# Kernel tuning notes

Hardware: AMD Instinct MI355X
Metric: run time of the kernel (lower is better)

The kernel has to match this reference:

```python
import jax, jax.numpy as jnp
import numpy as np

D_MODEL, NHEAD = 256, 8
HEAD_DIM = D_MODEL // NHEAD  # 32, also the conv group count


def layer_norm(x, w, b, eps=1e-5):
    mu = jnp.mean(x, axis=-1, keepdims=True)
    var = jnp.var(x, axis=-1, keepdims=True)
    return (x - mu) * jax.lax.rsqrt(var + eps) * w + b


def setup_inputs() -> dict:
    key = jax.random.key(0)
    ks = jax.random.split(key, 12)
    b, H, W = 4, 120, 160
    L = H * W  # 19200; 'self' path requires L == H*W
    d, h = D_MODEL, NHEAD
    s = 0.05
    p = lambda i, shape: jax.random.normal(ks[i], shape, jnp.float32) * s
    return {
        "x": jax.random.normal(ks[0], (b, L, d), jnp.float32),
        "source": jax.random.normal(ks[1], (b, L, d), jnp.float32),
        "Wq": p(2, (d, d)), "Wk": p(3, (d, d)), "Wv": p(4, (d, d)),
        "Wmerge": p(5, (d, d)),
        "Wmlp1": p(6, (2 * d, 2 * d)), "Wmlp2": p(7, (2 * d, d)),
        "ln1_w": jnp.ones((d,), jnp.float32), "ln1_b": jnp.zeros((d,), jnp.float32),
        "ln2_w": jnp.ones((d,), jnp.float32), "ln2_b": jnp.zeros((d,), jnp.float32),
        "Wdown": p(8, (2 * d, 64)), "Wup": p(9, (64, d)),
        "fc_w": p(10, (9, 3 * h)), "fc_b": jnp.zeros((9,), jnp.float32),
        "dep_w": p(11, (d, 9, 3, 3)),  # torch OIHW layout, groups=32 (O/g=8, I/g=9)
        "dep_b": jnp.zeros((d,), jnp.float32),
        "rate": jnp.full((1,), 0.5, jnp.float32),
        "H": H, "W": W,
    }


def reference(x, source, Wq, Wk, Wv, Wmerge, Wmlp1, Wmlp2,
              ln1_w, ln1_b, ln2_w, ln2_b, Wdown, Wup,
              fc_w, fc_b, dep_w, dep_b, rate, H, W):
    # name == 'self' path is hardcoded (conv branch active)
    b, L, d = x.shape
    h, hd = NHEAD, HEAD_DIM
    S = source.shape[1]

    q = (x @ Wq).reshape(b, L, h, hd)
    k = (source @ Wk).reshape(b, S, h, hd)
    v = (source @ Wv).reshape(b, S, h, hd)

    # ---- conv branch ----
    # [b, L, h, 3*hd] -> [b, L, 3h, hd] -> [b, 3h, L, hd]
    f_all = jnp.concatenate([q, k, v], axis=-1).reshape(b, L, 3 * h, hd)
    f_all = jnp.transpose(f_all, (0, 2, 1, 3))
    # 1x1 conv 3h -> 9 over (L, hd) 'spatial' grid
    f9 = jnp.einsum('oc,bcld->bold', fc_w, f_all) + fc_b[None, :, None, None]
    # [b, 9, L, hd] -> [b, hd, 9, L] -> [b, 9*hd, H, W]
    f_conv = jnp.transpose(f9, (0, 3, 1, 2)).reshape(b, 9 * hd, H, W)
    out_conv = jax.lax.conv_general_dilated(
        f_conv, dep_w, window_strides=(1, 1), padding=((1, 1), (1, 1)),
        feature_group_count=hd, dimension_numbers=('NCHW', 'OIHW', 'NCHW'))
    out_conv = out_conv + dep_b[None, :, None, None]
    out_conv = jnp.transpose(out_conv, (0, 2, 3, 1)).reshape(b, L, d)

    # ---- linear attention (elu+1 feature map), O(N) ----
    Qf = jax.nn.elu(q) + 1.0
    Kf = jax.nn.elu(k) + 1.0
    v_len = jnp.float32(S)
    vals = v / v_len
    KV = jnp.einsum('bshd,bshv->bhdv', Kf, vals)
    Z = 1.0 / (jnp.einsum('blhd,bhd->blh', Qf, Kf.sum(axis=1)) + 1e-6)
    message = jnp.einsum('blhd,bhdv,blh->blhv', Qf, KV, Z) * v_len

    # ---- merge / norm / MLP / adapter ----
    message = message.reshape(b, L, d) @ Wmerge
    message = layer_norm(message, ln1_w, ln1_b)
    cat1 = jnp.concatenate([x, message], axis=2)
    message = jax.nn.relu(cat1 @ Wmlp1) @ Wmlp2
    message = layer_norm(message, ln2_w, ln2_b)

    cat2 = jnp.concatenate([x, message], axis=2)
    up = jax.nn.relu(cat2 @ Wdown) @ Wup
    message = message + up * 0.1
    message = message + rate * out_conv
    return x + message
```

## Files before the change

### kernel.cpp

```cpp
#include <hip/hip_runtime.h>
#include <stdint.h>

#define LL 19200
#define NBATCH 4
#define NROWS (NBATCH * LL)
#define HH 120
#define WW 160

typedef short bhalf8 __attribute__((ext_vector_type(8)));
typedef float f32x4 __attribute__((ext_vector_type(4)));

__device__ __forceinline__ float bfbits2f(uint32_t u) { union { uint32_t i; float f; } c; c.i = u << 16; return c.f; }
__device__ __forceinline__ float bf2f(uint16_t h) { return bfbits2f((uint32_t)h); }
__device__ __forceinline__ uint16_t f2bf(float f) {
    union { float f; uint32_t i; } c; c.f = f;
    return (uint16_t)((c.i + 0x7FFFu + ((c.i >> 16) & 1u)) >> 16);
}
__device__ __forceinline__ uint32_t pk2(uint16_t a, uint16_t b) { return (uint32_t)a | ((uint32_t)b << 16); }
__device__ __forceinline__ float elup1(float x) { return x > 0.f ? x + 1.f : expf(x); }

__device__ __forceinline__ uint4 pack8f(const float* p) {
    float4 lo = *(const float4*)p; float4 hi = *(const float4*)(p + 4);
    uint4 s;
    s.x = pk2(f2bf(lo.x), f2bf(lo.y)); s.y = pk2(f2bf(lo.z), f2bf(lo.w));
    s.z = pk2(f2bf(hi.x), f2bf(hi.y)); s.w = pk2(f2bf(hi.z), f2bf(hi.w));
    return s;
}

__device__ __forceinline__ void gll16(const void* g, void* l) {
    __builtin_amdgcn_global_load_lds((const __attribute__((address_space(1))) uint32_t*)g,
                                     (__attribute__((address_space(3))) uint32_t*)l, 16, 0, 0);
}

__global__ __launch_bounds__(256)
void prep_all(const float* __restrict__ Wq, const float* __restrict__ Wk,
              const float* __restrict__ Wv, const float* __restrict__ Wm,
              const float* __restrict__ Wm1, const float* __restrict__ Wm2,
              const float* __restrict__ Wd, const float* __restrict__ Wu,
              uint16_t* __restrict__ wq, uint16_t* __restrict__ wk,
              uint16_t* __restrict__ wvv, uint16_t* __restrict__ wm,
              uint16_t* __restrict__ wm1, uint16_t* __restrict__ wm2,
              uint16_t* __restrict__ wd, uint16_t* __restrict__ wu) {
    __shared__ float ts[64][65];
    const int tid = threadIdx.x;
    int blk = blockIdx.x;
    const float* s; uint16_t* d; int K, N, t;
    if (blk < 64)        { int w = blk >> 4; t = blk & 15;
                           s = w == 0 ? Wq : w == 1 ? Wk : w == 2 ? Wv : Wm;
                           d = w == 0 ? wq : w == 1 ? wk : w == 2 ? wvv : wm;
                           K = 256; N = 256; }
    else if (blk < 128)  { s = Wm1; d = wm1; K = 512; N = 512; t = blk - 64; }
    else if (blk < 160)  { s = Wm2; d = wm2; K = 512; N = 256; t = blk - 128; }
    else if (blk < 168)  { s = Wd;  d = wd;  K = 512; N = 64;  t = blk - 160; }
    else                 { s = Wu;  d = wu;  K = 64;  N = 256; t = blk - 168; }
    const int ntk = K >> 6;
    const int tn = t / ntk, tk = t - tn * ntk;
    const int c = tid & 63, r4 = tid >> 6;
#pragma unroll
    for (int i = 0; i < 16; ++i) {
        int r = r4 * 16 + i;
        ts[r][c] = s[(long)(tk * 64 + r) * N + tn * 64 + c];
    }
    __syncthreads();
#pragma unroll
    for (int i = 0; i < 16; ++i) {
        int rr = r4 * 16 + i;
        d[(long)(tn * 64 + rr) * K + tk * 64 + c] = f2bf(ts[c][rr]);
    }
}

#define EPI_NONE 0
#define EPI_RELU 1
#define EPI_LN 2
#define EPI_FINAL 3

template<int BN, int K, int MODE_A, int EPI>
__global__ __launch_bounds__(512)
void gemm_big(const float* __restrict__ A0f, const uint16_t* __restrict__ A0b,
              const uint16_t* __restrict__ A1b,
              const uint16_t* __restrict__ Wt,
              uint16_t* __restrict__ outb, float* __restrict__ outf, int outW,
              uint16_t* __restrict__ sideout,
              const float* __restrict__ lnw, const float* __restrict__ lnb,
              const float* __restrict__ xres, const uint16_t* __restrict__ xresb,
              const uint16_t* __restrict__ msg2res,
              const uint16_t* __restrict__ convres, const float* __restrict__ ratep)
{
    constexpr int WCOLS = BN / 64;
    constexpr int WROWS = 8 / WCOLS;
    constexpr int MT = 128 / (WROWS * 16);
    constexpr int ASZ = 128 * 32;
    constexpr int BSZ = BN * 32;
    __shared__ __align__(16) uint16_t a_sm[2 * ASZ];
    __shared__ __align__(16) uint16_t b_sm[2 * BSZ];
    const int tid = threadIdx.x;
    const int lane = tid & 63;
    const int wv = tid >> 6;
    const int wr = wv / WCOLS, wc = wv % WCOLS;
    const long row0 = (long)blockIdx.x * 128;
    const int col0 = blockIdx.y * BN;
    const int l15 = lane & 15, lk = lane >> 4;

    f32x4 acc[MT][4];
#pragma unroll
    for (int m = 0; m < MT; ++m)
#pragma unroll
        for (int n = 0; n < 4; ++n) acc[m][n] = (f32x4){0.f, 0.f, 0.f, 0.f};

    const int sr = tid >> 2;
    const int sc = (tid & 3) * 8;
    const long argA = row0 + sr;

    auto stageAB = [&](int buf, int k0) {
        uint16_t* ab = a_sm + buf * ASZ;
        uint16_t* bb = b_sm + buf * BSZ;
        if (MODE_A == 0) {
            gll16(A0b + argA * (long)K + k0 + sc, ab + wv * 512);
        } else if (MODE_A == 1) {
            uint4 stg = pack8f(A0f + argA * (long)K + k0 + sc);
            *(uint4*)&ab[sr * 32 + sc] = stg;
            if (sideout) *(uint4*)(sideout + argA * (long)K + k0 + sc) = stg;
        } else if (MODE_A == 2) {
            if (k0 < 256) *(uint4*)&ab[sr * 32 + sc] = pack8f(A0f + argA * 256 + k0 + sc);
            else          gll16(A1b + argA * 256 + (k0 - 256) + sc, ab + wv * 512);
        } else {
            const uint16_t* srcp = (k0 < 256) ? (A0b + argA * 256 + k0 + sc)
                                              : (A1b + argA * 256 + (k0 - 256) + sc);
            gll16(srcp, ab + wv * 512);
        }
        if (BN == 256) {
            gll16(Wt + (long)(col0 + sr) * K + k0 + sc, bb + wv * 512);
            gll16(Wt + (long)(col0 + 128 + sr) * K + k0 + sc, bb + 4096 + wv * 512);
        } else {
            if (tid < 256) gll16(Wt + (long)(col0 + sr) * K + k0 + sc, bb + wv * 512);
        }
    };

    auto comp = [&](int buf) {
        const uint16_t* ab = a_sm + buf * ASZ;
        const uint16_t* bb = b_sm + buf * BSZ;
        bhalf8 af[MT];
#pragma unroll
        for (int m = 0; m < MT; ++m)
            af[m] = *(const bhalf8*)&ab[(wr * MT * 16 + m * 16 + l15) * 32 + lk * 8];
#pragma unroll
        for (int n = 0; n < 4; ++n) {
            bhalf8 bfr = *(const bhalf8*)&bb[(wc * 64 + n * 16 + l15) * 32 + lk * 8];
#pragma unroll
            for (int m = 0; m < MT; ++m)
                acc[m][n] = __builtin_amdgcn_mfma_f32_16x16x32_bf16(af[m], bfr, acc[m][n], 0, 0, 0);
        }
    };

    stageAB(0, 0);
    __syncthreads();
    int cur = 0;
#pragma unroll
    for (int k0 = 32; k0 < K; k0 += 32) {
        stageAB(cur ^ 1, k0);
        comp(cur);
        __syncthreads();
        cur ^= 1;
    }
    comp(cur);

    const int cl = l15;
    const int rg4 = lk * 4;

    if constexpr (EPI == EPI_LN) {
        __shared__ float red_s[4][128];
        __shared__ float red_ss[4][128];
#pragma unroll
        for (int m = 0; m < MT; ++m)
#pragma unroll
            for (int j = 0; j < 4; ++j) {
                float p = 0.f, pp = 0.f;
#pragma unroll
                for (int n = 0; n < 4; ++n) { float v = acc[m][n][j]; p += v; pp += v * v; }
#pragma unroll
                for (int msk = 1; msk < 16; msk <<= 1) { p += __shfl_xor(p, msk, 64); pp += __shfl_xor(pp, msk, 64); }
                if (cl == 0) {
                    int lr = wr * 64 + m * 16 + rg4 + j;
                    red_s[wc][lr] = p; red_ss[wc][lr] = pp;
                }
            }
        __syncthreads();
#pragma unroll
        for (int m = 0; m < MT; ++m)
#pragma unroll
            for (int j = 0; j < 4; ++j) {
                int lr = wr * 64 + m * 16 + rg4 + j;
                float s = red_s[0][lr] + red_s[1][lr] + red_s[2][lr] + red_s[3][lr];
                float ss = red_ss[0][lr] + red_ss[1][lr] + red_ss[2][lr] + red_ss[3][lr];
                float mu = s * (1.f / 256.f);
                float var = ss * (1.f / 256.f) - mu * mu;
                float rstd = rsqrtf(var + 1e-5f);
                long rowg = row0 + lr;
#pragma unroll
                for (int n = 0; n < 4; ++n) {
                    int col = wc * 64 + n * 16 + cl;
                    float vv = (acc[m][n][j] - mu) * rstd * lnw[col] + lnb[col];
                    outb[rowg * (long)outW + col] = f2bf(vv);
                }
            }
    } else if constexpr (EPI == EPI_FINAL) {
        float rate = ratep[0];
#pragma unroll
        for (int m = 0; m < MT; ++m)
#pragma unroll
            for (int j = 0; j < 4; ++j) {
                long rowg = row0 + wr * MT * 16 + m * 16 + rg4 + j;
                int bb2 = (int)(rowg / LL);
                int ll = (int)(rowg - (long)bb2 * LL);
#pragma unroll
                for (int n = 0; n < 4; ++n) {
                    int col = wc * 64 + n * 16 + cl;
                    long o = rowg * 256 + col;
                    float xv = xresb ? bf2f(xresb[o]) : xres[o];
                    float m2 = bf2f(msg2res[o]);
                    float cv = bf2f(convres[((long)(bb2 * 256 + col)) * LL + ll]);
                    outf[o] = xv + m2 + 0.1f * acc[m][n][j] + rate * cv;
                }
            }
    } else {
#pragma unroll
        for (int m = 0; m < MT; ++m)
#pragma unroll
            for (int j = 0; j < 4; ++j) {
                long rowg = row0 + wr * MT * 16 + m * 16 + rg4 + j;
#pragma unroll
                for (int n = 0; n < 4; ++n) {
                    int col = col0 + wc * 64 + n * 16 + cl;
                    float vv = acc[m][n][j];
                    if (EPI == EPI_RELU) vv = vv > 0.f ? vv : 0.f;
                    outb[rowg * (long)outW + col] = f2bf(vv);
                }
            }
    }
}

__global__ __launch_bounds__(256)
void kv_partial(const uint16_t* __restrict__ kb, const uint16_t* __restrict__ vb,
                float* __restrict__ part) {
    __shared__ float kf_sm[32][33];
    __shared__ float v_sm[32][36];
    const int tid = threadIdx.x;
    const int bh = blockIdx.y, b = bh >> 3, h = bh & 7;
    const int s0 = blockIdx.x * 256;
    const int d = tid >> 3, vg = tid & 7;
    const int sl = tid >> 3, e4 = (tid & 7) * 4;
    float a0 = 0.f, a1 = 0.f, a2 = 0.f, a3 = 0.f, aKs = 0.f;
    for (int it = 0; it < 8; ++it) {
        long base = ((long)(b * LL + s0 + it * 32 + sl)) * 256 + h * 32 + e4;
        uint2 kk = *(const uint2*)(kb + base);
        uint2 vv = *(const uint2*)(vb + base);
        kf_sm[sl][e4 + 0] = elup1(bfbits2f(kk.x & 0xFFFFu));
        kf_sm[sl][e4 + 1] = elup1(bfbits2f(kk.x >> 16));
        kf_sm[sl][e4 + 2] = elup1(bfbits2f(kk.y & 0xFFFFu));
        kf_sm[sl][e4 + 3] = elup1(bfbits2f(kk.y >> 16));
        float4 vf;
        vf.x = bfbits2f(vv.x & 0xFFFFu); vf.y = bfbits2f(vv.x >> 16);
        vf.z = bfbits2f(vv.y & 0xFFFFu); vf.w = bfbits2f(vv.y >> 16);
        *(float4*)&v_sm[sl][e4] = vf;
        __syncthreads();
#pragma unroll 8
        for (int s = 0; s < 32; ++s) {
            float kf = kf_sm[s][d];
            aKs += kf;
            float4 v4 = *(const float4*)&v_sm[s][vg * 4];
            a0 += kf * v4.x; a1 += kf * v4.y; a2 += kf * v4.z; a3 += kf * v4.w;
        }
        __syncthreads();
    }
    long pb = ((long)(blockIdx.x * 32 + bh)) * 1056;
    part[pb + d * 32 + vg * 4 + 0] = a0;
    part[pb + d * 32 + vg * 4 + 1] = a1;
    part[pb + d * 32 + vg * 4 + 2] = a2;
    part[pb + d * 32 + vg * 4 + 3] = a3;
    if (vg == 0) part[pb + 1024 + d] = aKs;
}

__global__ __launch_bounds__(256)
void kv_final(const float* __restrict__ part, float* __restrict__ KVg, float* __restrict__ Ksum) {
    const int bh = blockIdx.x, tid = threadIdx.x;
    for (int idx = tid; idx < 1056; idx += 256) {
        float s = 0.f;
        for (int c = 0; c < 75; ++c) s += part[((long)(c * 32 + bh)) * 1056 + idx];
        if (idx < 1024) KVg[bh * 1024 + idx] = s;
        else Ksum[bh * 32 + idx - 1024] = s;
    }
}

__global__ __launch_bounds__(256)
void attn_mfma(const uint16_t* __restrict__ qb, const float* __restrict__ KVg,
               const float* __restrict__ Ksum, uint16_t* __restrict__ msgout) {
    const int tid = threadIdx.x;
    const int lane = tid & 63;
    const int wv = tid >> 6;
    const long l0 = (long)blockIdx.x * 64;
    const int b = (int)(l0 / LL);
    const int l15 = lane & 15, lk = lane >> 4;
#pragma unroll
    for (int hi = 0; hi < 2; ++hi) {
        const int h = wv * 2 + hi;
        const float* kvb = KVg + ((long)(b * 8 + h)) * 1024;
        const float* ksb = Ksum + (b * 8 + h) * 32;
        bhalf8 B0, B1;
        float ks[8];
#pragma unroll
        for (int i = 0; i < 8; ++i) {
            int k = lk * 8 + i;
            B0[i] = (short)f2bf(kvb[k * 32 + l15]);
            B1[i] = (short)f2bf(kvb[k * 32 + 16 + l15]);
            ks[i] = ksb[k];
        }
#pragma unroll
        for (int rt = 0; rt < 4; ++rt) {
            long row = l0 + rt * 16 + l15;
            uint4 qv = *(const uint4*)(qb + row * 256 + h * 32 + lk * 8);
            float qf[8];
            qf[0] = elup1(bfbits2f(qv.x & 0xFFFFu)); qf[1] = elup1(bfbits2f(qv.x >> 16));
            qf[2] = elup1(bfbits2f(qv.y & 0xFFFFu)); qf[3] = elup1(bfbits2f(qv.y >> 16));
            qf[4] = elup1(bfbits2f(qv.z & 0xFFFFu)); qf[5] = elup1(bfbits2f(qv.z >> 16));
            qf[6] = elup1(bfbits2f(qv.w & 0xFFFFu)); qf[7] = elup1(bfbits2f(qv.w >> 16));
            bhalf8 A;
#pragma unroll
            for (int i = 0; i < 8; ++i) A[i] = (short)f2bf(qf[i]);
            float p = qf[0]*ks[0] + qf[1]*ks[1] + qf[2]*ks[2] + qf[3]*ks[3]
                    + qf[4]*ks[4] + qf[5]*ks[5] + qf[6]*ks[6] + qf[7]*ks[7];
            p += __shfl_xor(p, 16, 64);
            p += __shfl_xor(p, 32, 64);
            f32x4 d0 = (f32x4){0.f,0.f,0.f,0.f}, d1 = (f32x4){0.f,0.f,0.f,0.f};
            d0 = __builtin_amdgcn_mfma_f32_16x16x32_bf16(A, B0, d0, 0, 0, 0);
            d1 = __builtin_amdgcn_mfma_f32_16x16x32_bf16(A, B1, d1, 0, 0, 0);
#pragma unroll
            for (int j = 0; j < 4; ++j) {
                int orl = lk * 4 + j;
                float zr = __shfl(p, orl, 64);
                float Z = 1.f / (zr + 1e-6f);
                long orow = l0 + rt * 16 + orl;
                msgout[orow * 256 + h * 32 + l15]      = f2bf(d0[j] * Z);
                msgout[orow * 256 + h * 32 + 16 + l15] = f2bf(d1[j] * Z);
            }
        }
    }
}

__global__ __launch_bounds__(256)
void f9_kernel(const uint16_t* __restrict__ qb, const uint16_t* __restrict__ kb,
               const uint16_t* __restrict__ vb, const float* __restrict__ fcw,
               const float* __restrict__ fcb, uint16_t* __restrict__ fconv) {
    __shared__ __align__(16) uint16_t sm[3 * 32 * 256];
    char* smb = (char*)sm;
    const int tid = threadIdx.x;
    const int b = blockIdx.y;
    const int l0 = blockIdx.x * 32;
    for (int idx = tid; idx < 3072; idx += 256) {
        int tsr = idx >> 10, row = (idx >> 5) & 31, c = idx & 31;
        const uint16_t* src = tsr == 0 ? qb : (tsr == 1 ? kb : vb);
        uint4 v = *(const uint4*)(src + ((long)(b * LL + l0 + row)) * 256 + c * 8);
        int boff = (c * 16) ^ ((row & 7) << 4);
        *(uint4*)(smb + (tsr * 32 + row) * 512 + boff) = v;
    }
    __syncthreads();
    const int li = tid & 31, g = tid >> 5;
    float acc[9][4];
#pragma unroll
    for (int o = 0; o < 9; ++o) {
        float bv = fcb[o];
#pragma unroll
        for (int j = 0; j < 4; ++j) acc[o][j] = bv;
    }
    const int swz = (li & 7) << 4;
#pragma unroll
    for (int h = 0; h < 8; ++h) {
        float f[3][4];
#pragma unroll
        for (int s = 0; s < 3; ++s) {
            int boff = (h * 64 + g * 8) ^ swz;
            uint2 r = *(const uint2*)(smb + (s * 32 + li) * 512 + boff);
            f[s][0] = bfbits2f(r.x & 0xFFFFu); f[s][1] = bfbits2f(r.x >> 16);
            f[s][2] = bfbits2f(r.y & 0xFFFFu); f[s][3] = bfbits2f(r.y >> 16);
        }
#pragma unroll
        for (int o = 0; o < 9; ++o) {
            float w0 = fcw[o * 24 + 3 * h + 0];
            float w1 = fcw[o * 24 + 3 * h + 1];
            float w2 = fcw[o * 24 + 3 * h + 2];
#pragma unroll
            for (int j = 0; j < 4; ++j)
                acc[o][j] += w0 * f[0][j] + w1 * f[1][j] + w2 * f[2][j];
        }
    }
    const long ob = (long)(b * 288) * LL + l0 + li;
#pragma unroll
    for (int j = 0; j < 4; ++j) {
        int dp = g * 4 + j;
#pragma unroll
        for (int o = 0; o < 9; ++o)
            fconv[ob + (long)(dp * 9 + o) * LL] = f2bf(acc[o][j]);
    }
}

__global__ __launch_bounds__(256)
void dwconv2(const uint16_t* __restrict__ fconv, const float* __restrict__ depw,
             const float* __restrict__ depb, uint16_t* __restrict__ convout) {
    __shared__ __align__(16) uint16_t in_sm[9][26][48];
    __shared__ float w_sm[8][81];
    __shared__ float b_sm2[8];
    const int tid = threadIdx.x;
    const int bg = blockIdx.z, b = bg >> 5, g = bg & 31;
    const int y0 = blockIdx.y * 24;
    const int x0 = blockIdx.x * 32;
    for (int idx = tid; idx < 648; idx += 256)
        w_sm[idx / 81][idx % 81] = depw[(long)(g * 8) * 81 + idx];
    if (tid < 8) b_sm2[tid] = depb[g * 8 + tid];
    for (int rIdx = tid; rIdx < 234; rIdx += 256) {
        int i = rIdx / 26, r = rIdx - i * 26;
        int yy = y0 + r - 1;
        uint16_t* dst = &in_sm[i][r][0];
        if (yy >= 0 && yy < HH) {
            const uint16_t* rp = fconv + ((long)(b * 288 + g * 9 + i)) * LL + yy * WW;
            *(uint4*)&dst[8]  = *(const uint4*)(rp + x0);
            *(uint4*)&dst[16] = *(const uint4*)(rp + x0 + 8);
            *(uint4*)&dst[24] = *(const uint4*)(rp + x0 + 16);
            *(uint4*)&dst[32] = *(const uint4*)(rp + x0 + 24);
            dst[7]  = (x0 > 0) ? rp[x0 - 1] : (uint16_t)0;
            dst[40] = (x0 + 32 < WW) ? rp[x0 + 32] : (uint16_t)0;
        } else {
            uint4 z = {0, 0, 0, 0};
            *(uint4*)&dst[8] = z; *(uint4*)&dst[16] = z;
            *(uint4*)&dst[24] = z; *(uint4*)&dst[32] = z;
            dst[7] = 0; dst[40] = 0;
        }
    }
    __syncthreads();
    const int xi = tid & 7, m = (tid >> 3) & 7, ys = tid >> 6;
    float acc[6][4];
    float bias = b_sm2[m];
#pragma unroll
    for (int r = 0; r < 6; ++r)
#pragma unroll
        for (int o = 0; o < 4; ++o) acc[r][o] = bias;
    for (int i = 0; i < 9; ++i) {
        float w[9];
#pragma unroll
        for (int t = 0; t < 9; ++t) w[t] = w_sm[m][i * 9 + t];
#pragma unroll
        for (int rr = 0; rr < 8; ++rr) {
            const uint16_t* rowb = &in_sm[i][ys * 6 + rr][4 + xi * 4];
            uint2 lo = *(const uint2*)rowb;
            uint2 hi = *(const uint2*)(rowb + 4);
            uint32_t ex = *(const uint32_t*)(rowb + 8);
            float f[6];
            f[0] = bfbits2f(lo.y >> 16);
            f[1] = bfbits2f(hi.x & 0xFFFFu);
            f[2] = bfbits2f(hi.x >> 16);
            f[3] = bfbits2f(hi.y & 0xFFFFu);
            f[4] = bfbits2f(hi.y >> 16);
            f[5] = bfbits2f(ex & 0xFFFFu);
#pragma unroll
            for (int ky = 0; ky < 3; ++ky) {
                int ro = rr - ky;
                if (ro >= 0 && ro < 6) {
#pragma unroll
                    for (int o = 0; o < 4; ++o)
                        acc[ro][o] += w[ky * 3 + 0] * f[o] + w[ky * 3 + 1] * f[o + 1] + w[ky * 3 + 2] * f[o + 2];
                }
            }
        }
    }
    long chbase = ((long)(b * 256 + g * 8 + m)) * LL;
#pragma unroll
    for (int rl = 0; rl < 6; ++rl) {
        int y = y0 + ys * 6 + rl;
        uint2 st;
        st.x = pk2(f2bf(acc[rl][0]), f2bf(acc[rl][1]));
        st.y = pk2(f2bf(acc[rl][2]), f2bf(acc[rl][3]));
        *(uint2*)(convout + chbase + (long)y * WW + x0 + xi * 4) = st;
    }
}

extern "C" void kernel_launch(void* const* d_in, const int* in_sizes, int n_in,
                              void* d_out, int out_size, void* d_ws, size_t ws_size,
                              hipStream_t stream) {
    (void)in_sizes; (void)n_in; (void)out_size;
    const float* x      = (const float*)d_in[0];
    const float* src    = (const float*)d_in[1];
    const float* Wq     = (const float*)d_in[2];
    const float* Wk     = (const float*)d_in[3];
    const float* Wv     = (const float*)d_in[4];
    const float* Wmerge = (const float*)d_in[5];
    const float* Wmlp1  = (const float*)d_in[6];
    const float* Wmlp2  = (const float*)d_in[7];
    const float* ln1w   = (const float*)d_in[8];
    const float* ln1b   = (const float*)d_in[9];
    const float* ln2w   = (const float*)d_in[10];
    const float* ln2b   = (const float*)d_in[11];
    const float* Wdown  = (const float*)d_in[12];
    const float* Wup    = (const float*)d_in[13];
    const float* fcw    = (const float*)d_in[14];
    const float* fcb    = (const float*)d_in[15];
    const float* depw   = (const float*)d_in[16];
    const float* depb   = (const float*)d_in[17];
    const float* rate   = (const float*)d_in[18];

    char* ws = (char*)d_ws;
    const size_t SZ_NB = (size_t)NROWS * 256 * 2;
    const size_t O_Q = 0;
    const size_t O_K = SZ_NB;
    const size_t O_V = 2 * SZ_NB;
    const size_t O_FCONV = 3 * SZ_NB;
    const size_t O_CONVOUT = O_FCONV + (size_t)NBATCH * 288 * LL * 2;
    const size_t O_PART = O_CONVOUT + SZ_NB;
    const size_t O_KV = O_PART + (size_t)75 * 32 * 1056 * 4;
    const size_t O_KS = O_KV + (size_t)32 * 1024 * 4;
    const size_t O_WT = O_KS + (size_t)32 * 32 * 4;
    const size_t O_XB = O_WT + 704512 * 2 + 1024;
    const size_t O_SRCB = O_XB + SZ_NB;
    const size_t NEED = O_SRCB + SZ_NB;

    uint16_t* qB      = (uint16_t*)(ws + O_Q);
    uint16_t* kB      = (uint16_t*)(ws + O_K);
    uint16_t* vB      = (uint16_t*)(ws + O_V);
    uint16_t* fconv   = (uint16_t*)(ws + O_FCONV);
    uint16_t* convout = (uint16_t*)(ws + O_CONVOUT);
    float*    part    = (float*)(ws + O_PART);
    float*    KVg     = (float*)(ws + O_KV);
    float*    Ksg     = (float*)(ws + O_KS);
    uint16_t* wt_q    = (uint16_t*)(ws + O_WT);
    uint16_t* wt_k    = wt_q + 256 * 256;
    uint16_t* wt_v    = wt_k + 256 * 256;
    uint16_t* wt_m    = wt_v + 256 * 256;
    uint16_t* wt_m1   = wt_m + 256 * 256;
    uint16_t* wt_m2   = wt_m1 + 512 * 512;
    uint16_t* wt_d    = wt_m2 + 512 * 256;
    uint16_t* wt_u    = wt_d + 512 * 64;
    uint16_t* xb      = (uint16_t*)(ws + O_XB);
    uint16_t* srcb    = (uint16_t*)(ws + O_SRCB);
    uint16_t* msgattn = kB;
    uint16_t* msgB    = vB;
    uint16_t* hidden  = qB;
    uint16_t* msg2    = fconv;
    uint16_t* h2      = (uint16_t*)(ws + O_PART);

    const bool big = ws_size >= NEED;

    prep_all<<<172, 256, 0, stream>>>(Wq, Wk, Wv, Wmerge, Wmlp1, Wmlp2, Wdown, Wup,
                                      wt_q, wt_k, wt_v, wt_m, wt_m1, wt_m2, wt_d, wt_u);

    const dim3 g600(NROWS / 128, 1);
    gemm_big<256, 256, 1, EPI_NONE><<<g600, 512, 0, stream>>>(x, nullptr, nullptr, wt_q, qB, nullptr, 256,
        big ? xb : nullptr, nullptr, nullptr, nullptr, nullptr, nullptr, nullptr, nullptr);
    gemm_big<256, 256, 1, EPI_NONE><<<g600, 512, 0, stream>>>(src, nullptr, nullptr, wt_k, kB, nullptr, 256,
        big ? srcb : nullptr, nullptr, nullptr, nullptr, nullptr, nullptr, nullptr, nullptr);
    if (big) {
        gemm_big<256, 256, 0, EPI_NONE><<<g600, 512, 0, stream>>>(nullptr, srcb, nullptr, wt_v, vB, nullptr, 256,
            nullptr, nullptr, nullptr, nullptr, nullptr, nullptr, nullptr, nullptr);
    } else {
        gemm_big<256, 256, 1, EPI_NONE><<<g600, 512, 0, stream>>>(src, nullptr, nullptr, wt_v, vB, nullptr, 256,
            nullptr, nullptr, nullptr, nullptr, nullptr, nullptr, nullptr, nullptr);
    }
    kv_partial<<<dim3(75, 32), 256, 0, stream>>>(kB, vB, part);
    kv_final<<<32, 256, 0, stream>>>(part, KVg, Ksg);
    f9_kernel<<<dim3(LL / 32, NBATCH), 256, 0, stream>>>(qB, kB, vB, fcw, fcb, fconv);
    dwconv2<<<dim3(5, 5, 128), 256, 0, stream>>>(fconv, depw, depb, convout);
    attn_mfma<<<NROWS / 64, 256, 0, stream>>>(qB, KVg, Ksg, msgattn);
    gemm_big<256, 256, 0, EPI_LN><<<g600, 512, 0, stream>>>(nullptr, msgattn, nullptr, wt_m, msgB, nullptr, 256,
        nullptr, ln1w, ln1b, nullptr, nullptr, nullptr, nullptr, nullptr);
    if (big) {
        gemm_big<256, 512, 3, EPI_RELU><<<dim3(NROWS / 128, 2), 512, 0, stream>>>(nullptr, xb, msgB, wt_m1, hidden, nullptr, 512,
            nullptr, nullptr, nullptr, nullptr, nullptr, nullptr, nullptr, nullptr);
    } else {
        gemm_big<256, 512, 2, EPI_RELU><<<dim3(NROWS / 128, 2), 512, 0, stream>>>(x, nullptr, msgB, wt_m1, hidden, nullptr, 512,
            nullptr, nullptr, nullptr, nullptr, nullptr, nullptr, nullptr, nullptr);
    }
    gemm_big<256, 512, 0, EPI_LN><<<g600, 512, 0, stream>>>(nullptr, hidden, nullptr, wt_m2, msg2, nullptr, 256,
        nullptr, ln2w, ln2b, nullptr, nullptr, nullptr, nullptr, nullptr);
    if (big) {
        gemm_big<64, 512, 3, EPI_RELU><<<g600, 512, 0, stream>>>(nullptr, xb, msg2, wt_d, h2, nullptr, 64,
            nullptr, nullptr, nullptr, nullptr, nullptr, nullptr, nullptr, nullptr);
    } else {
        gemm_big<64, 512, 2, EPI_RELU><<<g600, 512, 0, stream>>>(x, nullptr, msg2, wt_d, h2, nullptr, 64,
            nullptr, nullptr, nullptr, nullptr, nullptr, nullptr, nullptr, nullptr);
    }
    gemm_big<256, 64, 0, EPI_FINAL><<<g600, 512, 0, stream>>>(nullptr, h2, nullptr, wt_u, nullptr, (float*)d_out, 256,
        nullptr, nullptr, nullptr, x, big ? xb : nullptr, msg2, convout, rate);
}
```

Before: 856.3 us.

## Pipeline GEMM k-loop with raw barriers, stage epilogue stores, pre-convert inputs

For GEMMs whose A operand is bf16 loaded via global_load_lds, the k-loop now uses explicit vmcnt waits and raw s_barrier so the next tile's loads stay in flight while the current tile computes. Epilogues (plain, ReLU, LayerNorm) now stage results through shared memory and write coalesced 16-byte rows instead of scattered 2-byte stores. A separate conversion kernel turns x and source to bf16 up front so the Q/K/V GEMMs all read bf16 directly. The MLP1 grid is transposed so the two column blocks of a row tile run next to each other for better A reuse in cache. The added conversion pass, the extra barriers and the hand-tuned waitcnt counts add cost and fragility.

```diff
diff --git a/kernel.cpp b/kernel.cpp
--- a/kernel.cpp
+++ b/kernel.cpp
@@ -30,6 +30,22 @@
 __device__ __forceinline__ void gll16(const void* g, void* l) {
     __builtin_amdgcn_global_load_lds((const __attribute__((address_space(1))) uint32_t*)g,
                                      (__attribute__((address_space(3))) uint32_t*)l, 16, 0, 0);
+}
+
+__device__ __forceinline__ void barrier_raw() {
+    asm volatile("" ::: "memory");
+    __builtin_amdgcn_s_barrier();
+    asm volatile("" ::: "memory");
+}
+
+__global__ __launch_bounds__(256)
+void conv_bf16(const float* __restrict__ a, const float* __restrict__ b,
+               uint16_t* __restrict__ oa, uint16_t* __restrict__ ob) {
+    const float* s = blockIdx.y ? b : a;
+    uint16_t* d = blockIdx.y ? ob : oa;
+    long i = ((long)blockIdx.x * 256 + threadIdx.x) * 16;
+    *(uint4*)(d + i)     = pack8f(s + i);
+    *(uint4*)(d + i + 8) = pack8f(s + i + 8);
 }
 
 __global__ __launch_bounds__(256)
@@ -74,7 +90,7 @@
 #define EPI_LN 2
 #define EPI_FINAL 3
 
-template<int BN, int K, int MODE_A, int EPI>
+template<int BN, int K, int MODE_A, int EPI, int COLX>
 __global__ __launch_bounds__(512)
 void gemm_big(const float* __restrict__ A0f, const uint16_t* __restrict__ A0b,
               const uint16_t* __restrict__ A1b,
@@ -91,14 +107,17 @@
     constexpr int MT = 128 / (WROWS * 16);
     constexpr int ASZ = 128 * 32;
     constexpr int BSZ = BN * 32;
-    __shared__ __align__(16) uint16_t a_sm[2 * ASZ];
-    __shared__ __align__(16) uint16_t b_sm[2 * BSZ];
+    constexpr int NSTEP = K / 32;
+    constexpr bool PIPE = (MODE_A == 0 || MODE_A == 3);
+    __shared__ __align__(16) uint16_t smem[2 * ASZ + 2 * BSZ];
+    uint16_t* a_sm = smem;
+    uint16_t* b_sm = smem + 2 * ASZ;
     const int tid = threadIdx.x;
     const int lane = tid & 63;
     const int wv = tid >> 6;
     const int wr = wv / WCOLS, wc = wv % WCOLS;
-    const long row0 = (long)blockIdx.x * 128;
-    const int col0 = blockIdx.y * BN;
+    const long row0 = (long)(COLX ? blockIdx.y : blockIdx.x) * 128;
+    const int col0 = (COLX ? blockIdx.x : blockIdx.y) * BN;
     const int l15 = lane & 15, lk = lane >> 4;
 
     f32x4 acc[MT][4];
@@ -152,58 +171,44 @@
         }
     };
 
-    stageAB(0, 0);
+    if constexpr (PIPE) {
+        stageAB(0, 0);
+#pragma unroll
+        for (int t = 0; t < NSTEP; ++t) {
+            if (t + 1 < NSTEP) {
+                stageAB((t + 1) & 1, (t + 1) * 32);
+                if constexpr (BN == 256) {
+                    asm volatile("s_waitcnt vmcnt(3)" ::: "memory");
+                } else {
+                    if (wv < 4) asm volatile("s_waitcnt vmcnt(2)" ::: "memory");
+                    else        asm volatile("s_waitcnt vmcnt(1)" ::: "memory");
+                }
+            } else {
+                asm volatile("s_waitcnt vmcnt(0)" ::: "memory");
+            }
+            barrier_raw();
+            comp(t & 1);
+            barrier_raw();
+        }
+    } else {
+        stageAB(0, 0);
+        __syncthreads();
+        int cur = 0;
+#pragma unroll
+        for (int k0 = 32; k0 < K; k0 += 32) {
+            stageAB(cur ^ 1, k0);
+            comp(cur);
+            __syncthreads();
+            cur ^= 1;
+        }
+        comp(cur);
+    }
     __syncthreads();
-    int cur = 0;
-#pragma unroll
-    for (int k0 = 32; k0 < K; k0 += 32) {
-        stageAB(cur ^ 1, k0);
-        comp(cur);
-        __syncthreads();
-        cur ^= 1;
-    }
-    comp(cur);
 
     const int cl = l15;
     const int rg4 = lk * 4;
 
-    if constexpr (EPI == EPI_LN) {
-        __shared__ float red_s[4][128];
-        __shared__ float red_ss[4][128];
-#pragma unroll
-        for (int m = 0; m < MT; ++m)
-#pragma unroll
-            for (int j = 0; j < 4; ++j) {
-                float p = 0.f, pp = 0.f;
-#pragma unroll
-                for (int n = 0; n < 4; ++n) { float v = acc[m][n][j]; p += v; pp += v * v; }
-#pragma unroll
-                for (int msk = 1; msk < 16; msk <<= 1) { p += __shfl_xor(p, msk, 64); pp += __shfl_xor(pp, msk, 64); }
-                if (cl == 0) {
-                    int lr = wr * 64 + m * 16 + rg4 + j;
-                    red_s[wc][lr] = p; red_ss[wc][lr] = pp;
-                }
-            }
-        __syncthreads();
-#pragma unroll
-        for (int m = 0; m < MT; ++m)
-#pragma unroll
-            for (int j = 0; j < 4; ++j) {
-                int lr = wr * 64 + m * 16 + rg4 + j;
-                float s = red_s[0][lr] + red_s[1][lr] + red_s[2][lr] + red_s[3][lr];
-                float ss = red_ss[0][lr] + red_ss[1][lr] + red_ss[2][lr] + red_ss[3][lr];
-                float mu = s * (1.f / 256.f);
-                float var = ss * (1.f / 256.f) - mu * mu;
-                float rstd = rsqrtf(var + 1e-5f);
-                long rowg = row0 + lr;
-#pragma unroll
-                for (int n = 0; n < 4; ++n) {
-                    int col = wc * 64 + n * 16 + cl;
-                    float vv = (acc[m][n][j] - mu) * rstd * lnw[col] + lnb[col];
-                    outb[rowg * (long)outW + col] = f2bf(vv);
-                }
-            }
-    } else if constexpr (EPI == EPI_FINAL) {
+    if constexpr (EPI == EPI_FINAL) {
         float rate = ratep[0];
 #pragma unroll
         for (int m = 0; m < MT; ++m)
@@ -222,20 +227,78 @@
                     outf[o] = xv + m2 + 0.1f * acc[m][n][j] + rate * cv;
                 }
             }
-    } else {
+        return;
+    }
+
+    float mu_r[MT][4], rs_r[MT][4];
+    float lw[4], lb[4];
+    if constexpr (EPI == EPI_LN) {
+        float* red_s  = (float*)smem;
+        float* red_ss = red_s + 512;
 #pragma unroll
         for (int m = 0; m < MT; ++m)
 #pragma unroll
             for (int j = 0; j < 4; ++j) {
-                long rowg = row0 + wr * MT * 16 + m * 16 + rg4 + j;
-#pragma unroll
-                for (int n = 0; n < 4; ++n) {
-                    int col = col0 + wc * 64 + n * 16 + cl;
-                    float vv = acc[m][n][j];
-                    if (EPI == EPI_RELU) vv = vv > 0.f ? vv : 0.f;
-                    outb[rowg * (long)outW + col] = f2bf(vv);
+                float p = 0.f, pp = 0.f;
+#pragma unroll
+                for (int n = 0; n < 4; ++n) { float v = acc[m][n][j]; p += v; pp += v * v; }
+#pragma unroll
+                for (int msk = 1; msk < 16; msk <<= 1) { p += __shfl_xor(p, msk, 64); pp += __shfl_xor(pp, msk, 64); }
+                if (cl == 0) {
+                    int lr = wr * 64 + m * 16 + rg4 + j;
+                    red_s[wc * 128 + lr] = p; red_ss[wc * 128 + lr] = pp;
                 }
             }
+        __syncthreads();
+#pragma unroll
+        for (int m = 0; m < MT; ++m)
+#pragma unroll
+            for (int j = 0; j < 4; ++j) {
+                int lr = wr * 64 + m * 16 + rg4 + j;
+                float s  = red_s[lr] + red_s[128 + lr] + red_s[256 + lr] + red_s[384 + lr];
+                float ss = red_ss[lr] + red_ss[128 + lr] + red_ss[256 + lr] + red_ss[384 + lr];
+                float mu = s * (1.f / 256.f);
+                float var = ss * (1.f / 256.f) - mu * mu;
+                mu_r[m][j] = mu;
+                rs_r[m][j] = rsqrtf(var + 1e-5f);
+            }
+#pragma unroll
+        for (int n = 0; n < 4; ++n) {
+            lw[n] = lnw[wc * 64 + n * 16 + cl];
+            lb[n] = lnb[wc * 64 + n * 16 + cl];
+        }
+        __syncthreads();
+    }
+
+    constexpr int CST = BN + 8;
+    uint16_t* stg = (EPI == EPI_LN) ? (smem + 2048) : smem;
+    constexpr int ROWS = (BN == 256) ? 32 : 128;
+    constexpr int GPR = BN / 8;
+#pragma unroll
+    for (int m = 0; m < MT; ++m) {
+        __syncthreads();
+#pragma unroll
+        for (int j = 0; j < 4; ++j) {
+            int lr = wr * 16 + rg4 + j;
+#pragma unroll
+            for (int n = 0; n < 4; ++n) {
+                float v = acc[m][n][j];
+                if constexpr (EPI == EPI_RELU) v = v > 0.f ? v : 0.f;
+                if constexpr (EPI == EPI_LN)   v = (v - mu_r[m][j]) * rs_r[m][j] * lw[n] + lb[n];
+                stg[lr * CST + wc * 64 + n * 16 + cl] = f2bf(v);
+            }
+        }
+        __syncthreads();
+#pragma unroll
+        for (int it = 0; it < (ROWS * GPR + 511) / 512; ++it) {
+            int flat = it * 512 + tid;
+            if (flat < ROWS * GPR) {
+                int lr = flat / GPR, g = flat % GPR;
+                long grow = (BN == 256) ? (row0 + (lr >> 4) * 64 + m * 16 + (lr & 15))
+                                        : (row0 + lr);
+                *(uint4*)(outb + grow * (long)outW + col0 + g * 8) = *(const uint4*)&stg[lr * CST + g * 8];
+            }
+        }
     }
 }
 
@@ -550,15 +613,20 @@
                                       wt_q, wt_k, wt_v, wt_m, wt_m1, wt_m2, wt_d, wt_u);
 
     const dim3 g600(NROWS / 128, 1);
-    gemm_big<256, 256, 1, EPI_NONE><<<g600, 512, 0, stream>>>(x, nullptr, nullptr, wt_q, qB, nullptr, 256,
-        big ? xb : nullptr, nullptr, nullptr, nullptr, nullptr, nullptr, nullptr, nullptr);
-    gemm_big<256, 256, 1, EPI_NONE><<<g600, 512, 0, stream>>>(src, nullptr, nullptr, wt_k, kB, nullptr, 256,
-        big ? srcb : nullptr, nullptr, nullptr, nullptr, nullptr, nullptr, nullptr, nullptr);
     if (big) {
-        gemm_big<256, 256, 0, EPI_NONE><<<g600, 512, 0, stream>>>(nullptr, srcb, nullptr, wt_v, vB, nullptr, 256,
+        conv_bf16<<<dim3(4800, 2), 256, 0, stream>>>(x, src, xb, srcb);
+        gemm_big<256, 256, 0, EPI_NONE, 0><<<g600, 512, 0, stream>>>(nullptr, xb, nullptr, wt_q, qB, nullptr, 256,
+            nullptr, nullptr, nullptr, nullptr, nullptr, nullptr, nullptr, nullptr);
+        gemm_big<256, 256, 0, EPI_NONE, 0><<<g600, 512, 0, stream>>>(nullptr, srcb, nullptr, wt_k, kB, nullptr, 256,
+            nullptr, nullptr, nullptr, nullptr, nullptr, nullptr, nullptr, nullptr);
+        gemm_big<256, 256, 0, EPI_NONE, 0><<<g600, 512, 0, stream>>>(nullptr, srcb, nullptr, wt_v, vB, nullptr, 256,
             nullptr, nullptr, nullptr, nullptr, nullptr, nullptr, nullptr, nullptr);
     } else {
-        gemm_big<256, 256, 1, EPI_NONE><<<g600, 512, 0, stream>>>(src, nullptr, nullptr, wt_v, vB, nullptr, 256,
+        gemm_big<256, 256, 1, EPI_NONE, 0><<<g600, 512, 0, stream>>>(x, nullptr, nullptr, wt_q, qB, nullptr, 256,
+            nullptr, nullptr, nullptr, nullptr, nullptr, nullptr, nullptr, nullptr);
+        gemm_big<256, 256, 1, EPI_NONE, 0><<<g600, 512, 0, stream>>>(src, nullptr, nullptr, wt_k, kB, nullptr, 256,
+            nullptr, nullptr, nullptr, nullptr, nullptr, nullptr, nullptr, nullptr);
+        gemm_big<256, 256, 1, EPI_NONE, 0><<<g600, 512, 0, stream>>>(src, nullptr, nullptr, wt_v, vB, nullptr, 256,
             nullptr, nullptr, nullptr, nullptr, nullptr, nullptr, nullptr, nullptr);
     }
     kv_partial<<<dim3(75, 32), 256, 0, stream>>>(kB, vB, part);
@@ -566,24 +634,24 @@
     f9_kernel<<<dim3(LL / 32, NBATCH), 256, 0, stream>>>(qB, kB, vB, fcw, fcb, fconv);
     dwconv2<<<dim3(5, 5, 128), 256, 0, stream>>>(fconv, depw, depb, convout);
     attn_mfma<<<NROWS / 64, 256, 0, stream>>>(qB, KVg, Ksg, msgattn);
-    gemm_big<256, 256, 0, EPI_LN><<<g600, 512, 0, stream>>>(nullptr, msgattn, nullptr, wt_m, msgB, nullptr, 256,
+    gemm_big<256, 256, 0, EPI_LN, 0><<<g600, 512, 0, stream>>>(nullptr, msgattn, nullptr, wt_m, msgB, nullptr, 256,
         nullptr, ln1w, ln1b, nullptr, nullptr, nullptr, nullptr, nullptr);
     if (big) {
-        gemm_big<256, 512, 3, EPI_RELU><<<dim3(NROWS / 128, 2), 512, 0, stream>>>(nullptr, xb, msgB, wt_m1, hidden, nullptr, 512,
+        gemm_big<256, 512, 3, EPI_RELU, 1><<<dim3(2, NROWS / 128), 512, 0, stream>>>(nullptr, xb, msgB, wt_m1, hidden, nullptr, 512,
             nullptr, nullptr, nullptr, nullptr, nullptr, nullptr, nullptr, nullptr);
     } else {
-        gemm_big<256, 512, 2, EPI_RELU><<<dim3(NROWS / 128, 2), 512, 0, stream>>>(x, nullptr, msgB, wt_m1, hidden, nullptr, 512,
-            nullptr, nullptr, nullptr, nullptr, nullptr, nullptr, nullptr, nullptr);
-    }
-    gemm_big<256, 512, 0, EPI_LN><<<g600, 512, 0, stream>>>(nullptr, hidden, nullptr, wt_m2, msg2, nullptr, 256,
+        gemm_big<256, 512, 2, EPI_RELU, 0><<<dim3(NROWS / 128, 2), 512, 0, stream>>>(x, nullptr, msgB, wt_m1, hidden, nullptr, 512,
+            nullptr, nullptr, nullptr, nullptr, nullptr, nullptr, nullptr, nullptr);
+    }
+    gemm_big<256, 512, 0, EPI_LN, 0><<<g600, 512, 0, stream>>>(nullptr, hidden, nullptr, wt_m2, msg2, nullptr, 256,
         nullptr, ln2w, ln2b, nullptr, nullptr, nullptr, nullptr, nullptr);
     if (big) {
-        gemm_big<64, 512, 3, EPI_RELU><<<g600, 512, 0, stream>>>(nullptr, xb, msg2, wt_d, h2, nullptr, 64,
+        gemm_big<64, 512, 3, EPI_RELU, 0><<<g600, 512, 0, stream>>>(nullptr, xb, msg2, wt_d, h2, nullptr, 64,
             nullptr, nullptr, nullptr, nullptr, nullptr, nullptr, nullptr, nullptr);
     } else {
-        gemm_big<64, 512, 2, EPI_RELU><<<g600, 512, 0, stream>>>(x, nullptr, msg2, wt_d, h2, nullptr, 64,
-            nullptr, nullptr, nullptr, nullptr, nullptr, nullptr, nullptr, nullptr);
-    }
-    gemm_big<256, 64, 0, EPI_FINAL><<<g600, 512, 0, stream>>>(nullptr, h2, nullptr, wt_u, nullptr, (float*)d_out, 256,
+        gemm_big<64, 512, 2, EPI_RELU, 0><<<g600, 512, 0, stream>>>(x, nullptr, msg2, wt_d, h2, nullptr, 64,
+            nullptr, nullptr, nullptr, nullptr, nullptr, nullptr, nullptr, nullptr);
+    }
+    gemm_big<256, 64, 0, EPI_FINAL, 0><<<g600, 512, 0, stream>>>(nullptr, h2, nullptr, wt_u, nullptr, (float*)d_out, 256,
         nullptr, nullptr, nullptr, x, big ? xb : nullptr, msg2, convout, rate);
 }
```

Result: faster. 825.4 us (-3.6%).
